# Kernel tuning notes

Hardware: AMD Instinct MI355X
Metric: run time of the kernel (lower is better)

Reference implementation:

```python
import jax, jax.numpy as jnp
import numpy as np
from jax import lax

SEGMENTS = 64
KERNEL = 5


def setup_inputs() -> dict:
    key = jax.random.key(0)
    k1, k2, k3 = jax.random.split(key, 3)
    B, S, F = 4, 4096, 1024
    A6 = 512 * 6
    inp = jax.random.normal(k1, (B, S, F), dtype=jnp.float32)
    W = jax.random.normal(k2, (A6, F), dtype=jnp.float32) * (1.0 / np.sqrt(F))
    b = jax.random.normal(k3, (A6,), dtype=jnp.float32) * 0.01
    return {"inp": inp, "W": W, "b": b}


def reference(inp, W, b):
    # Fused projection: [B,S,F] @ [F,6A] -> [B,S,6A]
    x = jnp.einsum('bsf,af->bsa', inp, W) + b
    qry, key, val, seg, loc, out = jnp.split(x, 6, axis=2)  # each [B,S,A]
    B, S, A = out.shape

    # Global aggregated attention branch
    agg = qry.mean(axis=1)                              # [B,A]
    scores = jnp.einsum('ba,bsa->bs', agg, key)         # [B,S]
    w = jax.nn.softmax(scores, axis=1)                  # [B,S]
    ctx = jnp.einsum('bs,bsa->ba', w, val)              # [B,A]
    aggregated = ctx[:, None, :] * out                  # [B,S,A]

    # Segment max-pool branch
    nseg = S // SEGMENTS
    seg4 = seg.reshape(B, nseg, SEGMENTS, A)
    seg_max = seg4.max(axis=2, keepdims=True)           # [B,nseg,1,A]
    segment_max_pooled = (seg_max * out.reshape(B, nseg, SEGMENTS, A)).reshape(B, S, A)

    # Local sliding-window max-pool branch (stride 1, pad KERNEL//2, -inf padding)
    pad = KERNEL // 2
    local_max_pooled = lax.reduce_window(
        loc, -jnp.inf, lax.max,
        window_dimensions=(1, KERNEL, 1),
        window_strides=(1, 1, 1),
        padding=((0, 0), (pad, pad), (0, 0)))           # [B,S,A]

    return aggregated + segment_max_pooled + local_max_pooled
```

## Files before the change

kernel.cpp:

```cpp
#include <hip/hip_runtime.h>
#include <hip/hip_bf16.h>
#include <stdint.h>

#define B_    4
#define S_    4096
#define F_    1024
#define A_    512
#define N3_   1536
#define M_    16384

#define BM    128
#define BN    192
#define BK    32
#define NT    (F_ / BK)
#define LDP2  130

typedef __attribute__((ext_vector_type(8))) __bf16 bf16x8;
typedef __attribute__((ext_vector_type(4))) float f32x4;

#define MFMA(a, b, c) __builtin_amdgcn_mfma_f32_16x16x32_bf16((a), (b), (c), 0, 0, 0)

__device__ __forceinline__ float bflo(unsigned int u) {
  union { unsigned int i; float f; } v; v.i = u << 16; return v.f;
}
__device__ __forceinline__ float bfhi(unsigned int u) {
  union { unsigned int i; float f; } v; v.i = u & 0xffff0000u; return v.f;
}
__device__ __forceinline__ float bf1(unsigned short u) {
  union { unsigned int i; float f; } v; v.i = ((unsigned int)u) << 16; return v.f;
}
__device__ __forceinline__ unsigned short bfc(float f) {
  return __builtin_bit_cast(unsigned short, __float2bfloat16(f));
}
__device__ __forceinline__ ushort4 cvt_bf4(float4 v) {
  ushort4 o;
  o.x = bfc(v.x); o.y = bfc(v.y); o.z = bfc(v.z); o.w = bfc(v.w);
  return o;
}

typedef __attribute__((address_space(3))) unsigned int lds_uint;
typedef const __attribute__((address_space(1))) unsigned int glob_uint;
__device__ __forceinline__ void lds_load16(const void* g, void* l) {
  __builtin_amdgcn_global_load_lds((glob_uint*)g, (lds_uint*)l, 16, 0, 0);
}

__global__ __launch_bounds__(256) void convert_mean_kernel(
    const float* __restrict__ inp, const float* __restrict__ W,
    unsigned short* __restrict__ inp_bf, unsigned short* __restrict__ w_bf,
    float* __restrict__ mu) {
  int blk = blockIdx.x;
  int t   = threadIdx.x;
  int r0  = blk * 32;
  int b   = r0 >> 12;
  float acc0 = 0.f, acc1 = 0.f, acc2 = 0.f, acc3 = 0.f;
  for (int r = 0; r < 32; r++) {
    size_t row = (size_t)(r0 + r);
    float4 v = ((const float4*)(inp + row * F_))[t];
    acc0 += v.x; acc1 += v.y; acc2 += v.z; acc3 += v.w;
    ((ushort4*)(inp_bf + row * F_))[t] = cvt_bf4(v);
  }
  atomicAdd(&mu[b * F_ + t * 4 + 0], acc0);
  atomicAdd(&mu[b * F_ + t * 4 + 1], acc1);
  atomicAdd(&mu[b * F_ + t * 4 + 2], acc2);
  atomicAdd(&mu[b * F_ + t * 4 + 3], acc3);

  const float* Wc = W + (size_t)N3_ * F_;
  const int n4 = (N3_ * F_) / 4;
  for (int i = blk * 256 + t; i < n4; i += 512 * 256) {
    ((ushort4*)w_bf)[i] = cvt_bf4(((const float4*)Wc)[i]);
  }
}

__global__ void agg_kernel(const float* __restrict__ mu, const float* __restrict__ W,
                           const float* __restrict__ bias, float* __restrict__ agg) {
  int gw = blockIdx.x * 4 + (threadIdx.x >> 6);
  int lane = threadIdx.x & 63;
  int b = gw >> 9, a = gw & 511;
  const float4* wr = (const float4*)(W + (size_t)a * F_);
  const float4* mr = (const float4*)(mu + b * F_);
  float s = 0.f;
#pragma unroll
  for (int k = 0; k < 4; k++) {
    float4 wv = wr[lane + 64 * k], mv = mr[lane + 64 * k];
    s += wv.x * mv.x + wv.y * mv.y + wv.z * mv.z + wv.w * mv.w;
  }
  for (int off = 32; off; off >>= 1) s += __shfl_down(s, off);
  if (lane == 0) agg[b * A_ + a] = s * (1.f / S_) + bias[a];
}

__global__ void v_kernel(const float* __restrict__ agg, const float* __restrict__ W,
                         float* __restrict__ v) {
  int fc = blockIdx.x;
  int ac = blockIdx.y;
  int t = threadIdx.x;
  int f = fc * 256 + t;
  const float* Wk = W + (size_t)A_ * F_;
  float s0 = 0.f, s1 = 0.f, s2 = 0.f, s3 = 0.f;
  int a0 = ac * 64;
  for (int a = a0; a < a0 + 64; a++) {
    float wv = Wk[(size_t)a * F_ + f];
    s0 += agg[a] * wv;
    s1 += agg[A_ + a] * wv;
    s2 += agg[2 * A_ + a] * wv;
    s3 += agg[3 * A_ + a] * wv;
  }
  atomicAdd(&v[f], s0);
  atomicAdd(&v[F_ + f], s1);
  atomicAdd(&v[2 * F_ + f], s2);
  atomicAdd(&v[3 * F_ + f], s3);
}

__global__ __launch_bounds__(256) void scores_u_kernel(
    const unsigned short* __restrict__ inp_bf, const float* __restrict__ v,
    float* __restrict__ uP, float* __restrict__ mlzl) {
  extern __shared__ char sulds[];
  unsigned short* xl = (unsigned short*)sulds;
  float* sc  = (float*)(sulds + 131072);
  float* wsl = sc + 64;

  int blk = blockIdx.x;
  int b = blk >> 6, ch = blk & 63;
  int s0 = ch * 64;
  int t = threadIdx.x, lane = t & 63, wv = t >> 6;

  const float4* vp = (const float4*)(v + b * F_);
  float4 va0 = vp[lane * 2], va1 = vp[lane * 2 + 1];
  float4 vb0 = vp[(lane + 64) * 2], vb1 = vp[(lane + 64) * 2 + 1];
#pragma unroll
  for (int i = 0; i < 16; i++) {
    int r = wv * 16 + i;
    const uint4* ip = (const uint4*)(inp_bf + ((size_t)(b * S_ + s0 + r)) * F_);
    uint4 x0 = ip[lane], x1 = ip[lane + 64];
    *(uint4*)&xl[r * 1024 + lane * 8]       = x0;
    *(uint4*)&xl[r * 1024 + 512 + lane * 8] = x1;
    float s = bflo(x0.x) * va0.x + bfhi(x0.x) * va0.y + bflo(x0.y) * va0.z + bfhi(x0.y) * va0.w +
              bflo(x0.z) * va1.x + bfhi(x0.z) * va1.y + bflo(x0.w) * va1.z + bfhi(x0.w) * va1.w +
              bflo(x1.x) * vb0.x + bfhi(x1.x) * vb0.y + bflo(x1.y) * vb0.z + bfhi(x1.y) * vb0.w +
              bflo(x1.z) * vb1.x + bfhi(x1.z) * vb1.y + bflo(x1.w) * vb1.z + bfhi(x1.w) * vb1.w;
    for (int off = 32; off; off >>= 1) s += __shfl_down(s, off);
    if (lane == 0) sc[r] = s;
  }
  __syncthreads();

  float m = -1e30f;
#pragma unroll
  for (int i = 0; i < 64; i++) m = fmaxf(m, sc[i]);
  if (t < 64) wsl[t] = __expf(sc[t] - m);
  __syncthreads();

  {
    const unsigned short* xp = xl + t * 4;
    float a0 = 0.f, a1 = 0.f, a2 = 0.f, a3 = 0.f;
    for (int s = 0; s < 64; s++) {
      uint2 xv = *(const uint2*)&xp[s * 1024];
      float w = wsl[s];
      a0 += w * bflo(xv.x); a1 += w * bfhi(xv.x);
      a2 += w * bflo(xv.y); a3 += w * bfhi(xv.y);
    }
    float4 o; o.x = a0; o.y = a1; o.z = a2; o.w = a3;
    *(float4*)&uP[(size_t)blk * 1024 + t * 4] = o;
  }
  if (t == 0) {
    float Z = 0.f;
#pragma unroll
    for (int i = 0; i < 64; i++) Z += wsl[i];
    mlzl[blk * 2] = m; mlzl[blk * 2 + 1] = Z;
  }
}

__global__ void ufin_kernel(const float* __restrict__ uP, const float* __restrict__ mlzl,
                            float* __restrict__ u) {
  int b = blockIdx.x >> 2, fs = blockIdx.x & 3;
  int f = fs * 256 + threadIdx.x;
  float M = -1e30f;
#pragma unroll
  for (int i = 0; i < 64; i++) M = fmaxf(M, mlzl[(b * 64 + i) * 2]);
  float Z = 0.f;
#pragma unroll
  for (int i = 0; i < 64; i++) Z += __expf(mlzl[(b * 64 + i) * 2] - M) * mlzl[(b * 64 + i) * 2 + 1];
  float acc = 0.f;
  for (int ch = 0; ch < 64; ch++) {
    float sc = __expf(mlzl[(b * 64 + ch) * 2] - M);
    acc += sc * uP[(size_t)(b * 64 + ch) * 1024 + f];
  }
  u[b * F_ + f] = acc / Z;
}

__global__ void ctx_kernel(const float* __restrict__ u, const float* __restrict__ W,
                           const float* __restrict__ bias, float* __restrict__ ctx) {
  int gw = blockIdx.x * 4 + (threadIdx.x >> 6);
  int lane = threadIdx.x & 63;
  int b = gw >> 9, a = gw & 511;
  const float4* wr = (const float4*)(W + (size_t)(2 * A_ + a) * F_);
  const float4* ur = (const float4*)(u + b * F_);
  float s = 0.f;
#pragma unroll
  for (int k = 0; k < 4; k++) {
    float4 wv = wr[lane + 64 * k], uv = ur[lane + 64 * k];
    s += wv.x * uv.x + wv.y * uv.y + wv.z * uv.z + wv.w * uv.w;
  }
  for (int off = 32; off; off >>= 1) s += __shfl_down(s, off);
  if (lane == 0) ctx[b * A_ + a] = s + bias[2 * A_ + a];
}

__global__ __launch_bounds__(512, 4) void gemm_fused(
    const __hip_bfloat16* __restrict__ Abf,
    const __hip_bfloat16* __restrict__ Wbf,
    const float* __restrict__ biasP,
    const float* __restrict__ ctx,
    float* __restrict__ out,
    unsigned short* __restrict__ sideLoc,
    float* __restrict__ sideGO) {
  extern __shared__ unsigned short smem[];
  unsigned short* ldsA = smem;
  unsigned short* ldsB = smem + 8192;
  unsigned short* Xt   = smem;
  float* segred = (float*)((char*)smem + 192 * LDP2 * 2);

  int bid = blockIdx.x;
  int swz = (bid & 7) * 128 + (bid >> 3);
  int mb = swz >> 3;
  int nb = swz & 7;

  int tid  = threadIdx.x;
  int lane = tid & 63;
  int wv   = tid >> 6;
  int wm   = wv >> 2;
  int wn   = wv & 3;
  int lo   = lane & 15, hi = lane >> 4;

  int rsw = ((hi ^ (lo & 3)) << 3);

  const __hip_bfloat16* Ab = Abf + (size_t)mb * BM * F_;

  int srow  = tid >> 2;
  int sslot = (((tid & 3) ^ (srow & 3)) << 3);
  size_t gB0 = (size_t)((srow >> 6) * 512 + nb * 64 + (srow & 63)) * F_;
  size_t gB1 = (size_t)(1024 + nb * 64 + (srow & 63)) * F_;

  f32x4 acc[4][3];
#pragma unroll
  for (int i = 0; i < 4; i++)
#pragma unroll
    for (int j = 0; j < 3; j++) acc[i][j] = (f32x4){0.f, 0.f, 0.f, 0.f};

  int aBase = (wm * 64 + lo) * 32;
  int bBase = (wn * 48 + lo) * 32;

#define STAGE(kt_, buf_)                                                                   \
  {                                                                                        \
    int kof_ = (kt_) * BK;                                                                 \
    lds_load16(Ab + (size_t)srow * F_ + kof_ + sslot, ldsA + (buf_) * 4096 + wv * 512);    \
    lds_load16(Wbf + gB0 + kof_ + sslot,              ldsB + (buf_) * 6144 + wv * 512);    \
    if (wv < 4)                                                                            \
      lds_load16(Wbf + gB1 + kof_ + sslot, ldsB + (buf_) * 6144 + 4096 + wv * 512);        \
  }

  STAGE(0, 0);

  for (int kt = 0; kt < NT; ++kt) {
    int c = kt & 1, nx = c ^ 1;
    bool pf = (kt + 1 < NT);
    const unsigned short* la = ldsA + c * 4096;
    const unsigned short* lb = ldsB + c * 6144;

    __builtin_amdgcn_s_barrier();
    if (pf) {
      STAGE(kt + 1, nx);
      if (wv < 4) asm volatile("s_waitcnt vmcnt(3)" ::: "memory");
      else        asm volatile("s_waitcnt vmcnt(2)" ::: "memory");
    } else {
      asm volatile("s_waitcnt vmcnt(0)" ::: "memory");
    }
    __builtin_amdgcn_s_barrier();

    bf16x8 af[4], bfr[3];
#pragma unroll
    for (int fi = 0; fi < 4; fi++) af[fi] = *(const bf16x8*)&la[aBase + fi * 512 + rsw];
#pragma unroll
    for (int fj = 0; fj < 3; fj++) bfr[fj] = *(const bf16x8*)&lb[bBase + fj * 512 + rsw];
    asm volatile("s_waitcnt lgkmcnt(0)" ::: "memory");
    __builtin_amdgcn_sched_barrier(0);
    __builtin_amdgcn_s_setprio(1);
#pragma unroll
    for (int fi = 0; fi < 4; fi++)
#pragma unroll
      for (int fj = 0; fj < 3; fj++)
        acc[fi][fj] = MFMA(af[fi], bfr[fj], acc[fi][fj]);
    __builtin_amdgcn_s_setprio(0);
  }
#undef STAGE

  __syncthreads();

  float bias_r[3];
#pragma unroll
  for (int fj = 0; fj < 3; fj++) {
    int cl = wn * 48 + fj * 16 + lo;
    bias_r[fj] = biasP[(cl >> 6) * 512 + nb * 64 + (cl & 63)];
  }
#pragma unroll
  for (int fi = 0; fi < 4; fi++) {
#pragma unroll
    for (int fj = 0; fj < 3; fj++) {
      int cl = wn * 48 + fj * 16 + lo;
      int r  = wm * 64 + fi * 16 + hi * 4;
      float v0 = acc[fi][fj][0] + bias_r[fj];
      float v1 = acc[fi][fj][1] + bias_r[fj];
      float v2 = acc[fi][fj][2] + bias_r[fj];
      float v3 = acc[fi][fj][3] + bias_r[fj];
      unsigned int u01 = (unsigned int)bfc(v0) | ((unsigned int)bfc(v1) << 16);
      unsigned int u23 = (unsigned int)bfc(v2) | ((unsigned int)bfc(v3) << 16);
      *(unsigned int*)&Xt[cl * LDP2 + r]     = u01;
      *(unsigned int*)&Xt[cl * LDP2 + r + 2] = u23;
    }
  }
  __syncthreads();

  if (tid < 128) {
    int seg = tid >> 6, c = tid & 63;
    int base = c * LDP2 + seg * 64;
    float m = -1e30f;
#pragma unroll
    for (int k = 0; k < 32; k++) {
      unsigned int uu = *(const unsigned int*)&Xt[base + 2 * k];
      m = fmaxf(m, fmaxf(bflo(uu), bfhi(uu)));
    }
    segred[seg * 64 + c] = m;
  }
  __syncthreads();

  {
    int c  = lane;
    int r0 = wv * 16;
    int b  = mb >> 5;
    int gcol = nb * 64 + c;
    float g = ctx[b * 512 + gcol] + segred[(r0 >> 6) * 64 + c];
    int lbase = (64 + c) * LDP2;
    int obase = (128 + c) * LDP2;
    float lw0 = bf1(Xt[lbase + max(r0 - 2, 0)]);
    float lw1 = bf1(Xt[lbase + max(r0 - 1, 0)]);
    float lw2 = bf1(Xt[lbase + r0]);
    float lw3 = bf1(Xt[lbase + r0 + 1]);
    size_t obase_g = ((size_t)(mb * BM + r0)) * 512 + gcol;
#pragma unroll
    for (int j = 0; j < 16; j++) {
      int rn = min(r0 + j + 2, 127);
      float lw4 = bf1(Xt[lbase + rn]);
      float lm = fmaxf(fmaxf(fmaxf(lw0, lw1), fmaxf(lw2, lw3)), lw4);
      float o = bf1(Xt[obase + r0 + j]);
      out[obase_g + (size_t)j * 512] = g * o + lm;
      lw0 = lw1; lw1 = lw2; lw2 = lw3; lw3 = lw4;
    }
  }

  if (tid < 256) {
    int rsel = tid >> 6, c = tid & 63;
    int r = (rsel < 2) ? rsel : (124 + rsel);
    int b = mb >> 5;
    float g = ctx[b * 512 + nb * 64 + c] + segred[(r >> 6) * 64 + c];
    float o = bf1(Xt[(128 + c) * LDP2 + r]);
    int gr = mb * 4 + rsel;
    sideLoc[gr * 512 + nb * 64 + c] = Xt[(64 + c) * LDP2 + r];
    sideGO[gr * 512 + nb * 64 + c]  = g * o;
  }
}

__global__ void fixup_kernel(const unsigned short* __restrict__ sideLoc,
                             const float* __restrict__ sideGO,
                             float* __restrict__ out) {
  int rb = blockIdx.x;
  int tb = rb & 31;
  int t = threadIdx.x;
  int rsel = t >> 6, cq = t & 63;
#pragma unroll
  for (int k = 0; k < 8; k++) {
    int c = cq * 8 + k;
    float miss;
    int rl;
    if (rsel == 0) {
      if (tb == 0) continue;
      miss = fmaxf(bf1(sideLoc[((rb - 1) * 4 + 2) * 512 + c]),
                   bf1(sideLoc[((rb - 1) * 4 + 3) * 512 + c]));
      rl = 0;
    } else if (rsel == 1) {
      if (tb == 0) continue;
      miss = bf1(sideLoc[((rb - 1) * 4 + 3) * 512 + c]);
      rl = 1;
    } else if (rsel == 2) {
      if (tb == 31) continue;
      miss = bf1(sideLoc[((rb + 1) * 4 + 0) * 512 + c]);
      rl = 126;
    } else {
      if (tb == 31) continue;
      miss = fmaxf(bf1(sideLoc[((rb + 1) * 4 + 0) * 512 + c]),
                   bf1(sideLoc[((rb + 1) * 4 + 1) * 512 + c]));
      rl = 127;
    }
    size_t oi = ((size_t)rb * BM + rl) * 512 + c;
    float cand = sideGO[(rb * 4 + rsel) * 512 + c] + miss;
    out[oi] = fmaxf(out[oi], cand);
  }
}

extern "C" void kernel_launch(void* const* d_in, const int* in_sizes, int n_in,
                              void* d_out, int out_size, void* d_ws, size_t ws_size,
                              hipStream_t stream) {
  const float* inp  = (const float*)d_in[0];
  const float* W    = (const float*)d_in[1];
  const float* bias = (const float*)d_in[2];
  float* out = (float*)d_out;
  char* ws = (char*)d_ws;

  const size_t INP_OFF  = 0;
  const size_t W_OFF    = 33554432;
  const size_t MU_OFF   = 36700160;
  const size_t U_OFF    = MU_OFF + 16384;
  const size_t V_OFF    = U_OFF + 16384;
  const size_t AGG_OFF  = V_OFF + 16384;
  const size_t CTX_OFF  = AGG_OFF + 8192;
  const size_t SL_OFF   = CTX_OFF + 8192;
  const size_t SG_OFF   = SL_OFF + 524288;
  const size_t UP_OFF   = SG_OFF + 1048576;
  const size_t ML_OFF   = UP_OFF + 1048576;

  unsigned short* inp_bf = (unsigned short*)(ws + INP_OFF);
  unsigned short* w_bf   = (unsigned short*)(ws + W_OFF);
  float* mu     = (float*)(ws + MU_OFF);
  float* u      = (float*)(ws + U_OFF);
  float* v      = (float*)(ws + V_OFF);
  float* agg    = (float*)(ws + AGG_OFF);
  float* ctx    = (float*)(ws + CTX_OFF);
  unsigned short* sideLoc = (unsigned short*)(ws + SL_OFF);
  float* sideGO = (float*)(ws + SG_OFF);
  float* uP     = (float*)(ws + UP_OFF);
  float* mlzl   = (float*)(ws + ML_OFF);

  hipFuncSetAttribute(reinterpret_cast<const void*>(gemm_fused),
                      hipFuncAttributeMaxDynamicSharedMemorySize, 50432);
  hipFuncSetAttribute(reinterpret_cast<const void*>(scores_u_kernel),
                      hipFuncAttributeMaxDynamicSharedMemorySize, 131584);

  hipMemsetAsync(ws + MU_OFF, 0, 3 * 16384, stream);
  convert_mean_kernel<<<512, 256, 0, stream>>>(inp, W, inp_bf, w_bf, mu);
  agg_kernel<<<512, 256, 0, stream>>>(mu, W, bias, agg);
  v_kernel<<<dim3(4, 8), 256, 0, stream>>>(agg, W, v);
  scores_u_kernel<<<256, 256, 131584, stream>>>(inp_bf, v, uP, mlzl);
  ufin_kernel<<<16, 256, 0, stream>>>(uP, mlzl, u);
  ctx_kernel<<<512, 256, 0, stream>>>(u, W, bias, ctx);
  gemm_fused<<<1024, 512, 50432, stream>>>((const __hip_bfloat16*)inp_bf,
                                           (const __hip_bfloat16*)w_bf,
                                           bias + 3 * A_, ctx, out, sideLoc, sideGO);
  fixup_kernel<<<128, 256, 0, stream>>>(sideLoc, sideGO, out);
}
```

Before: 134.6 us.

## Double BK in GEMM with interleaved staged loads, and drop LDS staging in scores kernel

The fused GEMM main loop now uses a K-tile of 64 with an 8-way XOR swizzle. Each iteration is split into three MFMA phases, one per N sub-tile, and the next tile's A and B global-to-LDS loads and the B fragment reads are interleaved between those phases. This is meant to hide load latency behind MFMA work and halve the number of K iterations. The cost is more LDS per block (81920 bytes), which may lower occupancy, and more barriers per iteration. Separately, scores_u_kernel no longer caches 64 rows in 128KB of LDS and instead re-reads them from global memory (likely L2-resident), which frees LDS so more blocks can run at once.

```diff
diff --git a/kernel.cpp b/kernel.cpp
--- a/kernel.cpp
+++ b/kernel.cpp
@@ -10,8 +10,7 @@
 #define M_    16384
 
 #define BM    128
-#define BN    192
-#define BK    32
+#define BK    64
 #define NT    (F_ / BK)
 #define LDP2  130
 
@@ -113,15 +112,12 @@
 __global__ __launch_bounds__(256) void scores_u_kernel(
     const unsigned short* __restrict__ inp_bf, const float* __restrict__ v,
     float* __restrict__ uP, float* __restrict__ mlzl) {
-  extern __shared__ char sulds[];
-  unsigned short* xl = (unsigned short*)sulds;
-  float* sc  = (float*)(sulds + 131072);
-  float* wsl = sc + 64;
-
   int blk = blockIdx.x;
   int b = blk >> 6, ch = blk & 63;
   int s0 = ch * 64;
   int t = threadIdx.x, lane = t & 63, wv = t >> 6;
+  __shared__ float sc[64];
+  __shared__ float wsl[64];
 
   const float4* vp = (const float4*)(v + b * F_);
   float4 va0 = vp[lane * 2], va1 = vp[lane * 2 + 1];
@@ -131,8 +127,6 @@
     int r = wv * 16 + i;
     const uint4* ip = (const uint4*)(inp_bf + ((size_t)(b * S_ + s0 + r)) * F_);
     uint4 x0 = ip[lane], x1 = ip[lane + 64];
-    *(uint4*)&xl[r * 1024 + lane * 8]       = x0;
-    *(uint4*)&xl[r * 1024 + 512 + lane * 8] = x1;
     float s = bflo(x0.x) * va0.x + bfhi(x0.x) * va0.y + bflo(x0.y) * va0.z + bfhi(x0.y) * va0.w +
               bflo(x0.z) * va1.x + bfhi(x0.z) * va1.y + bflo(x0.w) * va1.z + bfhi(x0.w) * va1.w +
               bflo(x1.x) * vb0.x + bfhi(x1.x) * vb0.y + bflo(x1.y) * vb0.z + bfhi(x1.y) * vb0.w +
@@ -149,10 +143,10 @@
   __syncthreads();
 
   {
-    const unsigned short* xp = xl + t * 4;
+    const unsigned short* xp = inp_bf + ((size_t)(b * S_ + s0)) * F_ + t * 4;
     float a0 = 0.f, a1 = 0.f, a2 = 0.f, a3 = 0.f;
     for (int s = 0; s < 64; s++) {
-      uint2 xv = *(const uint2*)&xp[s * 1024];
+      uint2 xv = *(const uint2*)&xp[(size_t)s * F_];
       float w = wsl[s];
       a0 += w * bflo(xv.x); a1 += w * bfhi(xv.x);
       a2 += w * bflo(xv.y); a3 += w * bfhi(xv.y);
@@ -213,7 +207,7 @@
     float* __restrict__ sideGO) {
   extern __shared__ unsigned short smem[];
   unsigned short* ldsA = smem;
-  unsigned short* ldsB = smem + 8192;
+  unsigned short* ldsB = smem + 16384;
   unsigned short* Xt   = smem;
   float* segred = (float*)((char*)smem + 192 * LDP2 * 2);
 
@@ -227,16 +221,16 @@
   int wv   = tid >> 6;
   int wm   = wv >> 2;
   int wn   = wv & 3;
-  int lo   = lane & 15, hi = lane >> 4;
-
-  int rsw = ((hi ^ (lo & 3)) << 3);
+  int lo   = lane & 15, hi = lane >> 4, sw = lane & 7;
+
+  int bir0 = (((hi * 16)      ^ (sw << 4)) >> 1);
+  int bir1 = (((64 + hi * 16) ^ (sw << 4)) >> 1);
 
   const __hip_bfloat16* Ab = Abf + (size_t)mb * BM * F_;
 
-  int srow  = tid >> 2;
-  int sslot = (((tid & 3) ^ (srow & 3)) << 3);
-  size_t gB0 = (size_t)((srow >> 6) * 512 + nb * 64 + (srow & 63)) * F_;
-  size_t gB1 = (size_t)(1024 + nb * 64 + (srow & 63)) * F_;
+  int srow = tid >> 3;
+  int sel  = ((tid & 7) ^ (srow & 7)) * 8;
+  int ldst = wv * 512;
 
   f32x4 acc[4][3];
 #pragma unroll
@@ -244,52 +238,88 @@
 #pragma unroll
     for (int j = 0; j < 3; j++) acc[i][j] = (f32x4){0.f, 0.f, 0.f, 0.f};
 
-  int aBase = (wm * 64 + lo) * 32;
-  int bBase = (wn * 48 + lo) * 32;
-
-#define STAGE(kt_, buf_)                                                                   \
-  {                                                                                        \
-    int kof_ = (kt_) * BK;                                                                 \
-    lds_load16(Ab + (size_t)srow * F_ + kof_ + sslot, ldsA + (buf_) * 4096 + wv * 512);    \
-    lds_load16(Wbf + gB0 + kof_ + sslot,              ldsB + (buf_) * 6144 + wv * 512);    \
-    if (wv < 4)                                                                            \
-      lds_load16(Wbf + gB1 + kof_ + sslot, ldsB + (buf_) * 6144 + 4096 + wv * 512);        \
-  }
-
-  STAGE(0, 0);
+  int aBase = (wm * 64 + lo) * 64;
+  int bBase = (wn * 48 + lo) * 64;
+
+#define STG_A(kt_, buf_, r_)                                                              \
+  lds_load16(Ab + (size_t)((r_) * 64 + srow) * F_ + (kt_) * BK + sel,                     \
+             ldsA + (buf_) * 8192 + (r_) * 4096 + ldst)
+#define STG_B(kt_, buf_, q_)                                                              \
+  lds_load16(Wbf + (size_t)((q_) * 512 + nb * 64 + srow) * F_ + (kt_) * BK + sel,         \
+             ldsB + (buf_) * 12288 + (q_) * 4096 + ldst)
+
+  bf16x8 af[4][2], b0[2], b1[2], b2[2];
+
+  STG_A(0, 0, 0); STG_A(0, 0, 1);
+  STG_B(0, 0, 0); STG_B(0, 0, 1); STG_B(0, 0, 2);
+  asm volatile("s_waitcnt vmcnt(0)" ::: "memory");
+  __builtin_amdgcn_s_barrier();
+#pragma unroll
+  for (int i = 0; i < 4; i++) {
+    af[i][0] = *(const bf16x8*)&ldsA[aBase + i * 1024 + bir0];
+    af[i][1] = *(const bf16x8*)&ldsA[aBase + i * 1024 + bir1];
+  }
+  b0[0] = *(const bf16x8*)&ldsB[bBase + bir0];
+  b0[1] = *(const bf16x8*)&ldsB[bBase + bir1];
 
   for (int kt = 0; kt < NT; ++kt) {
     int c = kt & 1, nx = c ^ 1;
     bool pf = (kt + 1 < NT);
-    const unsigned short* la = ldsA + c * 4096;
-    const unsigned short* lb = ldsB + c * 6144;
-
-    __builtin_amdgcn_s_barrier();
-    if (pf) {
-      STAGE(kt + 1, nx);
-      if (wv < 4) asm volatile("s_waitcnt vmcnt(3)" ::: "memory");
-      else        asm volatile("s_waitcnt vmcnt(2)" ::: "memory");
-    } else {
-      asm volatile("s_waitcnt vmcnt(0)" ::: "memory");
-    }
-    __builtin_amdgcn_s_barrier();
-
-    bf16x8 af[4], bfr[3];
-#pragma unroll
-    for (int fi = 0; fi < 4; fi++) af[fi] = *(const bf16x8*)&la[aBase + fi * 512 + rsw];
-#pragma unroll
-    for (int fj = 0; fj < 3; fj++) bfr[fj] = *(const bf16x8*)&lb[bBase + fj * 512 + rsw];
+    const unsigned short* lb  = ldsB + c * 12288;
+    const unsigned short* lan = ldsA + nx * 8192;
+    const unsigned short* lbn = ldsB + nx * 12288;
+
+    if (pf) { STG_A(kt + 1, nx, 0); STG_A(kt + 1, nx, 1); }
     asm volatile("s_waitcnt lgkmcnt(0)" ::: "memory");
     __builtin_amdgcn_sched_barrier(0);
     __builtin_amdgcn_s_setprio(1);
 #pragma unroll
-    for (int fi = 0; fi < 4; fi++)
-#pragma unroll
-      for (int fj = 0; fj < 3; fj++)
-        acc[fi][fj] = MFMA(af[fi], bfr[fj], acc[fi][fj]);
+    for (int i = 0; i < 4; i++) {
+      acc[i][0] = MFMA(af[i][0], b0[0], acc[i][0]);
+      acc[i][0] = MFMA(af[i][1], b0[1], acc[i][0]);
+    }
     __builtin_amdgcn_s_setprio(0);
-  }
-#undef STAGE
+    b1[0] = *(const bf16x8*)&lb[bBase + 1024 + bir0];
+    b1[1] = *(const bf16x8*)&lb[bBase + 1024 + bir1];
+    __builtin_amdgcn_s_barrier();
+
+    if (pf) { STG_B(kt + 1, nx, 0); STG_B(kt + 1, nx, 1); STG_B(kt + 1, nx, 2); }
+    asm volatile("s_waitcnt lgkmcnt(0)" ::: "memory");
+    __builtin_amdgcn_sched_barrier(0);
+    __builtin_amdgcn_s_setprio(1);
+#pragma unroll
+    for (int i = 0; i < 4; i++) {
+      acc[i][1] = MFMA(af[i][0], b1[0], acc[i][1]);
+      acc[i][1] = MFMA(af[i][1], b1[1], acc[i][1]);
+    }
+    __builtin_amdgcn_s_setprio(0);
+    b2[0] = *(const bf16x8*)&lb[bBase + 2048 + bir0];
+    b2[1] = *(const bf16x8*)&lb[bBase + 2048 + bir1];
+    __builtin_amdgcn_s_barrier();
+
+    asm volatile("s_waitcnt lgkmcnt(0)" ::: "memory");
+    __builtin_amdgcn_sched_barrier(0);
+    __builtin_amdgcn_s_setprio(1);
+#pragma unroll
+    for (int i = 0; i < 4; i++) {
+      acc[i][2] = MFMA(af[i][0], b2[0], acc[i][2]);
+      acc[i][2] = MFMA(af[i][1], b2[1], acc[i][2]);
+    }
+    __builtin_amdgcn_s_setprio(0);
+    if (pf) asm volatile("s_waitcnt vmcnt(0)" ::: "memory");
+    __builtin_amdgcn_s_barrier();
+    if (pf) {
+#pragma unroll
+      for (int i = 0; i < 4; i++) {
+        af[i][0] = *(const bf16x8*)&lan[aBase + i * 1024 + bir0];
+        af[i][1] = *(const bf16x8*)&lan[aBase + i * 1024 + bir1];
+      }
+      b0[0] = *(const bf16x8*)&lbn[bBase + bir0];
+      b0[1] = *(const bf16x8*)&lbn[bBase + bir1];
+    }
+  }
+#undef STG_A
+#undef STG_B
 
   __syncthreads();
 
@@ -437,18 +467,16 @@
   float* mlzl   = (float*)(ws + ML_OFF);
 
   hipFuncSetAttribute(reinterpret_cast<const void*>(gemm_fused),
-                      hipFuncAttributeMaxDynamicSharedMemorySize, 50432);
-  hipFuncSetAttribute(reinterpret_cast<const void*>(scores_u_kernel),
-                      hipFuncAttributeMaxDynamicSharedMemorySize, 131584);
+                      hipFuncAttributeMaxDynamicSharedMemorySize, 81920);
 
   hipMemsetAsync(ws + MU_OFF, 0, 3 * 16384, stream);
   convert_mean_kernel<<<512, 256, 0, stream>>>(inp, W, inp_bf, w_bf, mu);
   agg_kernel<<<512, 256, 0, stream>>>(mu, W, bias, agg);
   v_kernel<<<dim3(4, 8), 256, 0, stream>>>(agg, W, v);
-  scores_u_kernel<<<256, 256, 131584, stream>>>(inp_bf, v, uP, mlzl);
+  scores_u_kernel<<<256, 256, 0, stream>>>(inp_bf, v, uP, mlzl);
   ufin_kernel<<<16, 256, 0, stream>>>(uP, mlzl, u);
   ctx_kernel<<<512, 256, 0, stream>>>(u, W, bias, ctx);
-  gemm_fused<<<1024, 512, 50432, stream>>>((const __hip_bfloat16*)inp_bf,
+  gemm_fused<<<1024, 512, 81920, stream>>>((const __hip_bfloat16*)inp_bf,
                                            (const __hip_bfloat16*)w_bf,
                                            bias + 3 * A_, ctx, out, sideLoc, sideGO);
   fixup_kernel<<<128, 256, 0, stream>>>(sideLoc, sideGO, out);
```

Result: faster. 127.0 us (-5.6%).
